# Optimization experiments

Measured on AMD Instinct MI355X. Metric: run time of the kernel, lower is better.

## Reference

```python
import jax, jax.numpy as jnp
import numpy as np

D = 512
H = 8
DK = D // H
EXP = 2
EPS = 1e-5


def _layernorm(x, g, b):
    mu = jnp.mean(x, axis=-1, keepdims=True)
    var = jnp.mean(jnp.square(x - mu), axis=-1, keepdims=True)
    return (x - mu) * jax.lax.rsqrt(var + EPS) * g + b


def setup_inputs() -> dict:
    key = jax.random.key(0)
    ks = jax.random.split(key, 10)
    B, C = 4, 2048
    s = 0.02
    return {
        "h": jax.random.normal(ks[0], (B, C, D), jnp.float32),
        "adj_bias": jax.random.normal(ks[1], (B, C, C), jnp.float32),
        "w_qkv": jax.random.normal(ks[2], (D, 3 * D), jnp.float32) * s,
        "b_qkv": jnp.zeros((3 * D,), jnp.float32),
        "w_out": jax.random.normal(ks[3], (D, D), jnp.float32) * s,
        "b_out": jnp.zeros((D,), jnp.float32),
        "ln1_g": jnp.ones((D,), jnp.float32),
        "ln1_b": jnp.zeros((D,), jnp.float32),
        "ln2_g": jnp.ones((D,), jnp.float32),
        "ln2_b": jnp.zeros((D,), jnp.float32),
        "w1": jax.random.normal(ks[4], (D, D * EXP), jnp.float32) * s,
        "b1": jnp.zeros((D * EXP,), jnp.float32),
        "w2": jax.random.normal(ks[5], (D * EXP, D), jnp.float32) * s,
        "b2": jnp.zeros((D,), jnp.float32),
    }


def reference(h, adj_bias, w_qkv, b_qkv, w_out, b_out, ln1_g, ln1_b, ln2_g, ln2_b, w1, b1, w2, b2):
    B, C, _ = h.shape
    scale = DK ** -0.5
    h_n = _layernorm(h, ln1_g, ln1_b)
    qkv = (h_n @ w_qkv + b_qkv).reshape(B, C, 3, H, DK)
    q, k, v = (qkv[:, :, i].transpose(0, 2, 1, 3) for i in range(3))  # (B,H,C,DK)
    logits = jnp.einsum('bhqd,bhkd->bhqk', q, k) * scale + adj_bias[:, None, :, :]
    attn = jax.nn.softmax(logits, axis=-1)  # (B,H,C,C); dropout off (eval)
    out = jnp.einsum('bhqk,bhkd->bhqd', attn, v).transpose(0, 2, 1, 3).reshape(B, C, D)
    h = h + out @ w_out + b_out
    ff = _layernorm(h, ln2_g, ln2_b)
    ff = jax.nn.gelu(ff @ w1 + b1, approximate=False) @ w2 + b2
    return h + ff
```

## Files before the change

### kernel.cpp

```cpp
#include <hip/hip_runtime.h>
#include <hip/hip_bf16.h>

#define BDIM 4
#define CDIM 2048
#define DDIM 512
#define HH   8
#define DKH  64
#define NROW (BDIM * CDIM)

typedef unsigned short u16;
typedef unsigned int   u32;
typedef u16   u16x4  __attribute__((ext_vector_type(4)));
typedef u16   u16x8  __attribute__((ext_vector_type(8)));
typedef u32   u32x4  __attribute__((ext_vector_type(4)));
typedef __bf16 bf16x8 __attribute__((ext_vector_type(8)));
typedef __bf16 bf16x2 __attribute__((ext_vector_type(2)));
typedef float f32x4  __attribute__((ext_vector_type(4)));
typedef float f32x16 __attribute__((ext_vector_type(16)));

#define LOG2E 1.4426950408889634f

__device__ __forceinline__ u16 f2bf(float f) {
  union { float f; unsigned u; } x; x.f = f;
  unsigned u = x.u;
  u += 0x7fffu + ((u >> 16) & 1u);
  return (u16)(u >> 16);
}
__device__ __forceinline__ float bf2f(u16 u) {
  return __builtin_bit_cast(float, (u32)u << 16);
}
__device__ __forceinline__ u32 pk2(float a, float b) {
  bf16x2 t; t[0] = (__bf16)a; t[1] = (__bf16)b;
  return __builtin_bit_cast(u32, t);
}
__device__ __forceinline__ float fexp2(float x) {
  float r;
  asm("v_exp_f32 %0, %1" : "=v"(r) : "v"(x));
  return r;
}

__device__ __forceinline__ void gload_lds16(const u16* gp, u16* lp) {
  __builtin_amdgcn_global_load_lds((__attribute__((address_space(1))) const void*)gp,
                                   (__attribute__((address_space(3))) void*)lp, 16, 0, 0);
}

__device__ __forceinline__ void ln_body(int bx, int tid,
                                        const float* __restrict__ x,
                                        const float* __restrict__ gamma,
                                        const float* __restrict__ beta,
                                        u16* __restrict__ y) {
  int gw = (bx * 256 + tid) >> 6;
  int l  = tid & 63;
  const float* xr = x + (size_t)gw * DDIM;
  float4 a = *(const float4*)(xr + l * 8);
  float4 b = *(const float4*)(xr + l * 8 + 4);
  float s = a.x + a.y + a.z + a.w + b.x + b.y + b.z + b.w;
  float q = a.x*a.x + a.y*a.y + a.z*a.z + a.w*a.w + b.x*b.x + b.y*b.y + b.z*b.z + b.w*b.w;
#pragma unroll
  for (int m = 1; m < 64; m <<= 1) { s += __shfl_xor(s, m); q += __shfl_xor(q, m); }
  float mu  = s * (1.0f / DDIM);
  float var = q * (1.0f / DDIM) - mu * mu;
  float rs  = rsqrtf(var + 1e-5f);
  float4 g0 = *(const float4*)(gamma + l * 8);
  float4 g1 = *(const float4*)(gamma + l * 8 + 4);
  float4 b0 = *(const float4*)(beta + l * 8);
  float4 b1 = *(const float4*)(beta + l * 8 + 4);
  u16x8 o;
  o[0] = f2bf((a.x - mu) * rs * g0.x + b0.x);
  o[1] = f2bf((a.y - mu) * rs * g0.y + b0.y);
  o[2] = f2bf((a.z - mu) * rs * g0.z + b0.z);
  o[3] = f2bf((a.w - mu) * rs * g0.w + b0.w);
  o[4] = f2bf((b.x - mu) * rs * g1.x + b1.x);
  o[5] = f2bf((b.y - mu) * rs * g1.y + b1.y);
  o[6] = f2bf((b.z - mu) * rs * g1.z + b1.z);
  o[7] = f2bf((b.w - mu) * rs * g1.w + b1.w);
  *(u16x8*)(y + (size_t)gw * DDIM + l * 8) = o;
}

__global__ __launch_bounds__(256) void ln_kernel(const float* __restrict__ x,
                                                 const float* __restrict__ gamma,
                                                 const float* __restrict__ beta,
                                                 u16* __restrict__ y) {
  ln_body(blockIdx.x, threadIdx.x, x, gamma, beta, y);
}

__global__ __launch_bounds__(256) void setup_kernel(const float* __restrict__ h,
                                                    const float* __restrict__ ln1g,
                                                    const float* __restrict__ ln1b,
                                                    u16* __restrict__ hn,
                                                    const float* __restrict__ adj,
                                                    u16* __restrict__ adjC,
                                                    const float* __restrict__ wqkv,
                                                    const float* __restrict__ wout,
                                                    const float* __restrict__ w1,
                                                    const float* __restrict__ w2,
                                                    u16* __restrict__ o_qkv,
                                                    u16* __restrict__ o_out,
                                                    u16* __restrict__ o_w1,
                                                    u16* __restrict__ o_w2) {
  const int bx = blockIdx.x;
  const int t = threadIdx.x;
  if (bx < 2048) {
    ln_body(bx, t, h, ln1g, ln1b, hn);
  } else if (bx < 3072) {
    const int f = bx - 2048;
    const int b = f >> 8, kt = (f >> 3) & 31;
    const int q0 = (f & 7) * 256;
    const int ch = t & 7, c16 = ch & 3, hi2 = ch >> 2, m = c16 >> 1;
    const int K0 = m * 32 + ((c16 * 2) & 3) * 8 + hi2 * 4;
#pragma unroll
    for (int itq = 0; itq < 8; ++itq) {
      int q = q0 + itq * 32 + (t >> 3);
      const float* src = adj + ((size_t)b * CDIM + q) * CDIM + kt * 64;
      f32x4 v0 = *(const f32x4*)(src + K0);
      f32x4 v1 = *(const f32x4*)(src + K0 + 8);
      u16x8 o;
      o[0] = f2bf(v0[0] * LOG2E); o[1] = f2bf(v0[1] * LOG2E);
      o[2] = f2bf(v0[2] * LOG2E); o[3] = f2bf(v0[3] * LOG2E);
      o[4] = f2bf(v1[0] * LOG2E); o[5] = f2bf(v1[1] * LOG2E);
      o[6] = f2bf(v1[2] * LOG2E); o[7] = f2bf(v1[3] * LOG2E);
      *(u16x8*)(adjC + ((size_t)(b * 32 + kt) * 2048 + q) * 64 + ch * 8) = o;
    }
  } else {
    int idx = (bx - 3072) * 256 + t;
    const float* w; u16* wt; int K, N;
    if (idx < 98304)       { w = wqkv; wt = o_qkv; K = 512;  N = 1536; }
    else if (idx < 131072) { idx -= 98304;  w = wout; wt = o_out; K = 512;  N = 512; }
    else if (idx < 196608) { idx -= 131072; w = w1;   wt = o_w1;  K = 512;  N = 1024; }
    else                   { idx -= 196608; w = w2;   wt = o_w2;  K = 1024; N = 512; }
    int kb = K >> 3;
    int n = idx / kb, k0 = (idx - n * kb) * 8;
    u16x8 o;
#pragma unroll
    for (int j = 0; j < 8; ++j) o[j] = f2bf(w[(size_t)(k0 + j) * N + n]);
    *(u16x8*)(wt + (size_t)n * K + k0) = o;
  }
}

template <int EPI>
__device__ __forceinline__ void gemm_epi(int row, int col, float val, int N,
                                         const float* __restrict__ res,
                                         float* __restrict__ outf,
                                         u16* __restrict__ outb,
                                         u16* __restrict__ outq,
                                         u16* __restrict__ outk,
                                         u16* __restrict__ outv) {
  if constexpr (EPI == 0) {
    int t = col >> 9, hh = (col >> 6) & 7, dk = col & 63;
    int bb = row >> 11, cc = row & 2047;
    if (t == 0) {
      val *= 0.125f * LOG2E;
      outq[(((size_t)bb * HH + hh) * CDIM + cc) * DKH + dk] = f2bf(val);
    } else if (t == 1) {
      outk[(((size_t)bb * HH + hh) * CDIM + cc) * DKH + dk] = f2bf(val);
    } else {
      outv[(((size_t)bb * HH + hh) * DKH + dk) * CDIM + cc] = f2bf(val);
    }
  } else if constexpr (EPI == 1) {
    size_t idx = (size_t)row * N + col;
    outf[idx] = val + res[idx];
  } else {
    float g = 0.5f * val * (1.0f + erff(val * 0.70710678118f));
    outb[(size_t)row * N + col] = f2bf(g);
  }
}

template <int EPI>
__global__ __launch_bounds__(256) void gemm128(const u16* __restrict__ A,
                                               const u16* __restrict__ Bt,
                                               const float* __restrict__ bias,
                                               const float* __restrict__ res,
                                               float* __restrict__ outf,
                                               u16* __restrict__ outb,
                                               u16* __restrict__ outq,
                                               u16* __restrict__ outk,
                                               u16* __restrict__ outv,
                                               int M, int N, int K) {
  __shared__ u16 As[2][128 * 64];
  __shared__ u16 Bs[2][128 * 64];
  const int tid = threadIdx.x;
  const int w = tid >> 6, l = tid & 63;
  const int l15 = l & 15, l4 = l >> 4, l7 = l15 & 7;
  const int bm = blockIdx.y, bn = blockIdx.x;
  const int wr = w >> 1, wc = w & 1;

  f32x4 acc[4][4] = {};

  const int sg = (l & 7) ^ (l >> 3);
  const u16* Ag = A  + (size_t)(bm * 128 + w * 32 + (l >> 3)) * K + sg * 8;
  const u16* Bg = Bt + (size_t)(bn * 128 + w * 32 + (l >> 3)) * K + sg * 8;

  auto stage = [&](int buf, int k0) {
#pragma unroll
    for (int i = 0; i < 4; ++i) {
      gload_lds16(Ag + (size_t)(8 * i) * K + k0, &As[buf][(w * 32 + 8 * i) * 64]);
      gload_lds16(Bg + (size_t)(8 * i) * K + k0, &Bs[buf][(w * 32 + 8 * i) * 64]);
    }
  };

  stage(0, 0);
  __syncthreads();
  int cur = 0;
  for (int k0 = 0; k0 < K; k0 += 64) {
    if (k0 + 64 < K) stage(cur ^ 1, k0 + 64);
#pragma unroll
    for (int s = 0; s < 2; ++s) {
      bf16x8 af[4], bf[4];
#pragma unroll
      for (int m = 0; m < 4; ++m)
        af[m] = *(const bf16x8*)(&As[cur][(wr * 64 + m * 16 + l15) * 64 + (((s * 4 + l4) ^ l7) * 8)]);
#pragma unroll
      for (int n = 0; n < 4; ++n)
        bf[n] = *(const bf16x8*)(&Bs[cur][(wc * 64 + n * 16 + l15) * 64 + (((s * 4 + l4) ^ l7) * 8)]);
#pragma unroll
      for (int m = 0; m < 4; ++m)
#pragma unroll
        for (int n = 0; n < 4; ++n)
          acc[m][n] = __builtin_amdgcn_mfma_f32_16x16x32_bf16(af[m], bf[n], acc[m][n], 0, 0, 0);
    }
    __syncthreads();
    cur ^= 1;
  }

#pragma unroll
  for (int m = 0; m < 4; ++m) {
    const int row0 = bm * 128 + wr * 64 + m * 16 + l4 * 4;
#pragma unroll
    for (int n = 0; n < 4; ++n) {
      const int col = bn * 128 + wc * 64 + n * 16 + l15;
      const float bv = bias[col];
#pragma unroll
      for (int r = 0; r < 4; ++r)
        gemm_epi<EPI>(row0 + r, col, acc[m][n][r] + bv, N, res, outf, outb, outq, outk, outv);
    }
  }
}

template <int EPI>
__global__ __launch_bounds__(256) void gemm64(const u16* __restrict__ A,
                                              const u16* __restrict__ Bt,
                                              const float* __restrict__ bias,
                                              const float* __restrict__ res,
                                              float* __restrict__ outf,
                                              u16* __restrict__ outb,
                                              u16* __restrict__ outq,
                                              u16* __restrict__ outk,
                                              u16* __restrict__ outv,
                                              int M, int N, int K) {
  __shared__ u16 As[2][64 * 64];
  __shared__ u16 Bs[2][128 * 64];
  const int tid = threadIdx.x;
  const int w = tid >> 6, l = tid & 63;
  const int l15 = l & 15, l4 = l >> 4, l7 = l15 & 7;
  const int bm = blockIdx.y, bn = blockIdx.x;

  f32x4 acc[4][2] = {};

  const int sg = (l & 7) ^ (l >> 3);
  const u16* Ag = A  + (size_t)(bm * 64  + w * 16 + (l >> 3)) * K + sg * 8;
  const u16* Bg = Bt + (size_t)(bn * 128 + w * 32 + (l >> 3)) * K + sg * 8;

  auto stage = [&](int buf, int k0) {
    gload_lds16(Ag + k0,                  &As[buf][(w * 16 + 0) * 64]);
    gload_lds16(Ag + (size_t)8 * K + k0,  &As[buf][(w * 16 + 8) * 64]);
    gload_lds16(Bg + k0,                  &Bs[buf][(w * 32 + 0) * 64]);
    gload_lds16(Bg + (size_t)8 * K + k0,  &Bs[buf][(w * 32 + 8) * 64]);
    gload_lds16(Bg + (size_t)16 * K + k0, &Bs[buf][(w * 32 + 16) * 64]);
    gload_lds16(Bg + (size_t)24 * K + k0, &Bs[buf][(w * 32 + 24) * 64]);
  };

  stage(0, 0);
  __syncthreads();
  int cur = 0;
  for (int k0 = 0; k0 < K; k0 += 64) {
    if (k0 + 64 < K) stage(cur ^ 1, k0 + 64);
#pragma unroll
    for (int s = 0; s < 2; ++s) {
      bf16x8 af[4], bf[2];
#pragma unroll
      for (int m = 0; m < 4; ++m)
        af[m] = *(const bf16x8*)(&As[cur][(m * 16 + l15) * 64 + (((s * 4 + l4) ^ l7) * 8)]);
#pragma unroll
      for (int n = 0; n < 2; ++n)
        bf[n] = *(const bf16x8*)(&Bs[cur][(w * 32 + n * 16 + l15) * 64 + (((s * 4 + l4) ^ l7) * 8)]);
#pragma unroll
      for (int m = 0; m < 4; ++m)
#pragma unroll
        for (int n = 0; n < 2; ++n)
          acc[m][n] = __builtin_amdgcn_mfma_f32_16x16x32_bf16(af[m], bf[n], acc[m][n], 0, 0, 0);
    }
    __syncthreads();
    cur ^= 1;
  }

#pragma unroll
  for (int m = 0; m < 4; ++m) {
    const int row0 = bm * 64 + m * 16 + l4 * 4;
#pragma unroll
    for (int n = 0; n < 2; ++n) {
      const int col = bn * 128 + w * 32 + n * 16 + l15;
      const float bv = bias[col];
#pragma unroll
      for (int r = 0; r < 4; ++r)
        gemm_epi<EPI>(row0 + r, col, acc[m][n][r] + bv, N, res, outf, outb, outq, outk, outv);
    }
  }
}

__global__ __launch_bounds__(512, 2) void flash_attn(const u16* __restrict__ Q,
                                                     const u16* __restrict__ Kg,
                                                     const u16* __restrict__ Vt,
                                                     const u16* __restrict__ adjC,
                                                     u16* __restrict__ O) {
  __shared__ u16 Ks[2][2][64 * 64];
  __shared__ u16 Vs[2][2][64 * 64];
  __shared__ float lw[4][32];
  __shared__ float lsx[4][32];
  const int flat = blockIdx.x + 16 * blockIdx.y;
  const int virt = (flat & 7) * 64 + (flat >> 3);
  const int qt = virt & 15;
  const int bh = virt >> 4;
  const int b = bh >> 3, hh = bh & 7;
  const int tid = threadIdx.x;
  const int w = tid >> 6, l = tid & 63;
  const int kh = w >> 2, qg = w & 3;
  const int q32 = l & 31, hi = l >> 5;
  const int qglob = qt * 128 + qg * 32 + q32;

  const u16* Qb = Q  + (size_t)bh * CDIM * DKH;
  const u16* Kb = Kg + (size_t)bh * CDIM * DKH;
  const u16* Vb = Vt + (size_t)bh * DKH * CDIM;

  const int srow = qg * 16 + (l >> 3);
  const int sg   = (l & 7) ^ (l >> 3);
  const u16* Kg0 = Kb + (size_t)(srow + 0) * DKH + sg * 8;
  const u16* Kg1 = Kb + (size_t)(srow + 8) * DKH + sg * 8;
  const u16* Vg0 = Vb + (size_t)(srow + 0) * CDIM + sg * 8;
  const u16* Vg1 = Vb + (size_t)(srow + 8) * CDIM + sg * 8;

  bf16x8 qf[4];
#pragma unroll
  for (int s = 0; s < 4; ++s)
    qf[s] = *(const bf16x8*)(Qb + (size_t)qglob * DKH + s * 16 + hi * 8);

  const u16* adjQ = adjC + ((size_t)(b * 32) * 2048 + qglob) * 64 + hi * 32;

  f32x16 oa[2] = {};
  float lsum = 0.f;

  auto stage = [&](int buf, int ktr) {
    int kta = kh * 16 + ktr;
    gload_lds16(Kg0 + (size_t)kta * 4096, &Ks[kh][buf][(qg * 16 + 0) * 64]);
    gload_lds16(Kg1 + (size_t)kta * 4096, &Ks[kh][buf][(qg * 16 + 8) * 64]);
    gload_lds16(Vg0 + kta * 64, &Vs[kh][buf][(qg * 16 + 0) * 64]);
    gload_lds16(Vg1 + kta * 64, &Vs[kh][buf][(qg * 16 + 8) * 64]);
  };
  auto ajload = [&](u16x8* dst, int ktr) {
    const u16* p = adjQ + (size_t)(kh * 16 + ktr) * 131072;
#pragma unroll
    for (int i = 0; i < 4; ++i) dst[i] = *(const u16x8*)(p + i * 8);
  };
  auto computeQK = [&](const u16* KsB, const u16x8* av, f32x16* sa) {
#pragma unroll
    for (int m = 0; m < 2; ++m)
#pragma unroll
      for (int r = 0; r < 16; ++r)
        sa[m][r] = bf2f(av[m * 2 + (r >> 3)][r & 7]);
    __builtin_amdgcn_s_setprio(1);
#pragma unroll
    for (int s = 0; s < 4; ++s)
#pragma unroll
      for (int m = 0; m < 2; ++m) {
        bf16x8 kf = *(const bf16x8*)(&KsB[(m * 32 + q32) * 64 + (((s * 2 + hi) ^ (q32 & 7)) * 8)]);
        sa[m] = __builtin_amdgcn_mfma_f32_32x32x16_bf16(kf, qf[s], sa[m], 0, 0, 0);
      }
    __builtin_amdgcn_s_setprio(0);
  };
  auto computePV = [&](const u16* VsB, f32x16* sa) {
#pragma unroll
    for (int m = 0; m < 2; ++m)
#pragma unroll
      for (int r = 0; r < 16; ++r) {
        float p = fexp2(sa[m][r]);
        sa[m][r] = p;
        lsum += p;
      }
    bf16x8 af[4];
#pragma unroll
    for (int m = 0; m < 2; ++m)
#pragma unroll
      for (int t2 = 0; t2 < 2; ++t2) {
        u32 w0 = pk2(sa[m][t2 * 8 + 0], sa[m][t2 * 8 + 1]);
        u32 w1 = pk2(sa[m][t2 * 8 + 2], sa[m][t2 * 8 + 3]);
        u32 w2 = pk2(sa[m][t2 * 8 + 4], sa[m][t2 * 8 + 5]);
        u32 w3 = pk2(sa[m][t2 * 8 + 6], sa[m][t2 * 8 + 7]);
        auto r02 = __builtin_amdgcn_permlane32_swap(w0, w2, false, false);
        auto r13 = __builtin_amdgcn_permlane32_swap(w1, w3, false, false);
        u32x4 aw;
        aw[0] = r02[0];
        aw[1] = r13[0];
        aw[2] = r02[1];
        aw[3] = r13[1];
        af[m * 2 + t2] = __builtin_bit_cast(bf16x8, aw);
      }
    __builtin_amdgcn_s_setprio(1);
#pragma unroll
    for (int s = 0; s < 4; ++s)
#pragma unroll
      for (int n = 0; n < 2; ++n) {
        bf16x8 vf = *(const bf16x8*)(&VsB[(n * 32 + q32) * 64 + (((s * 2 + hi) ^ (q32 & 7)) * 8)]);
        oa[n] = __builtin_amdgcn_mfma_f32_32x32x16_bf16(af[s], vf, oa[n], 0, 0, 0);
      }
    __builtin_amdgcn_s_setprio(0);
  };

  u16x8 avA[4], avB[4];
  f32x16 sa[2];
  stage(0, 0);
  ajload(avA, 0);
  __syncthreads();
#pragma unroll 1
  for (int it = 0; it < 8; ++it) {
    int ktr = it * 2;
    stage(1, ktr + 1);
    computeQK(&Ks[kh][0][0], avA, sa);
    ajload(avB, ktr + 1);
    computePV(&Vs[kh][0][0], sa);
    __syncthreads();
    if (ktr + 2 < 16) stage(0, ktr + 2);
    computeQK(&Ks[kh][1][0], avB, sa);
    if (ktr + 2 < 16) ajload(avA, ktr + 2);
    computePV(&Vs[kh][1][0], sa);
    __syncthreads();
  }

  lsum += __shfl_xor(lsum, 32);

  float* cb = (float*)&Vs[0][0][0];
  if (kh == 1) {
#pragma unroll
    for (int n = 0; n < 2; ++n)
#pragma unroll
      for (int r = 0; r < 16; ++r)
        cb[((qg * 2 + n) * 16 + r) * 64 + l] = oa[n][r];
    if (hi == 0) lsx[qg][q32] = lsum;
  }
  __syncthreads();
  if (kh == 0) {
    lsum += lsx[qg][q32];
#pragma unroll
    for (int n = 0; n < 2; ++n)
#pragma unroll
      for (int r = 0; r < 16; ++r)
        oa[n][r] += cb[((qg * 2 + n) * 16 + r) * 64 + l];
    lw[qg][q32] = 1.0f / lsum;
#pragma unroll
    for (int n = 0; n < 2; ++n)
#pragma unroll
      for (int r = 0; r < 16; ++r) {
        int qloc = (r & 3) + 8 * (r >> 2) + 4 * hi;
        int row = qt * 128 + qg * 32 + qloc;
        float val = oa[n][r] * lw[qg][qloc];
        O[((size_t)b * CDIM + row) * DDIM + hh * 64 + n * 32 + q32] = f2bf(val);
      }
  }
}

extern "C" void kernel_launch(void* const* d_in, const int* in_sizes, int n_in,
                              void* d_out, int out_size, void* d_ws, size_t ws_size,
                              hipStream_t stream) {
  const float* h      = (const float*)d_in[0];
  const float* adj    = (const float*)d_in[1];
  const float* w_qkv  = (const float*)d_in[2];
  const float* b_qkv  = (const float*)d_in[3];
  const float* w_out  = (const float*)d_in[4];
  const float* b_out  = (const float*)d_in[5];
  const float* ln1g   = (const float*)d_in[6];
  const float* ln1b   = (const float*)d_in[7];
  const float* ln2g   = (const float*)d_in[8];
  const float* ln2b   = (const float*)d_in[9];
  const float* w1     = (const float*)d_in[10];
  const float* b1     = (const float*)d_in[11];
  const float* w2     = (const float*)d_in[12];
  const float* b2     = (const float*)d_in[13];
  float* out = (float*)d_out;

  char* ws = (char*)d_ws;
  u16* adjC  = (u16*)(ws);
  u16* hn    = (u16*)(ws + 33554432);
  u16* qb    = (u16*)(ws + 41943040);
  u16* kb    = (u16*)(ws + 50331648);
  u16* vt    = (u16*)(ws + 58720256);
  u16* attn  = (u16*)(ws + 67108864);
  u16* wqkvt = (u16*)(ws + 75497472);
  u16* woutt = (u16*)(ws + 77070336);
  u16* w1t   = (u16*)(ws + 77594624);
  u16* w2t   = (u16*)(ws + 78643200);
  u16* ffin  = hn;
  u16* ffmid = qb;

  setup_kernel<<<4096, 256, 0, stream>>>(h, ln1g, ln1b, hn, adj, adjC,
                                         w_qkv, w_out, w1, w2,
                                         wqkvt, woutt, w1t, w2t);

  gemm128<0><<<dim3(12, 64), 256, 0, stream>>>(hn, wqkvt, b_qkv, nullptr,
                                               nullptr, nullptr, qb, kb, vt,
                                               NROW, 3 * DDIM, DDIM);

  flash_attn<<<dim3(16, 32), 512, 0, stream>>>(qb, kb, vt, adjC, attn);

  gemm64<1><<<dim3(4, 128), 256, 0, stream>>>(attn, woutt, b_out, h,
                                              out, nullptr, nullptr, nullptr, nullptr,
                                              NROW, DDIM, DDIM);

  ln_kernel<<<2048, 256, 0, stream>>>(out, ln2g, ln2b, ffin);

  gemm128<2><<<dim3(8, 64), 256, 0, stream>>>(ffin, w1t, b1, nullptr,
                                              nullptr, ffmid, nullptr, nullptr, nullptr,
                                              NROW, 2 * DDIM, DDIM);

  gemm64<1><<<dim3(4, 128), 256, 0, stream>>>(ffmid, w2t, b2, out,
                                              out, nullptr, nullptr, nullptr, nullptr,
                                              NROW, DDIM, 2 * DDIM);
}
```

Before: 192.4 us.

## Drop split-K in flash attention and add XCD-aware block remap to GEMMs

The attention kernel no longer splits the key range across two wave groups. Each 256-thread block now walks all 32 key tiles itself, which removes the cross-half LDS reduction and the extra barrier, halves shared memory, and raises the occupancy target. The normalisation factor is broadcast with a shuffle instead of going through LDS. Separately, the GEMM kernels remap block indices so that neighbouring tiles land on the same XCD for better L2 reuse. The trade-off is half as many waves per block and a longer serial loop per block.

```diff
diff --git a/kernel.cpp b/kernel.cpp
--- a/kernel.cpp
+++ b/kernel.cpp
@@ -165,6 +165,15 @@
   }
 }
 
+__device__ __forceinline__ void xcd_remap(int& bn, int& bm) {
+  int nbn = gridDim.x;
+  int nwg = nbn * gridDim.y;
+  int flat = blockIdx.x + nbn * blockIdx.y;
+  int virt = (flat & 7) * (nwg >> 3) + (flat >> 3);
+  bn = virt % nbn;
+  bm = virt / nbn;
+}
+
 template <int EPI>
 __global__ __launch_bounds__(256) void gemm128(const u16* __restrict__ A,
                                                const u16* __restrict__ Bt,
@@ -181,7 +190,8 @@
   const int tid = threadIdx.x;
   const int w = tid >> 6, l = tid & 63;
   const int l15 = l & 15, l4 = l >> 4, l7 = l15 & 7;
-  const int bm = blockIdx.y, bn = blockIdx.x;
+  int bn, bm;
+  xcd_remap(bn, bm);
   const int wr = w >> 1, wc = w & 1;
 
   f32x4 acc[4][4] = {};
@@ -252,7 +262,8 @@
   const int tid = threadIdx.x;
   const int w = tid >> 6, l = tid & 63;
   const int l15 = l & 15, l4 = l >> 4, l7 = l15 & 7;
-  const int bm = blockIdx.y, bn = blockIdx.x;
+  int bn, bm;
+  xcd_remap(bn, bm);
 
   f32x4 acc[4][2] = {};
 
@@ -307,15 +318,13 @@
   }
 }
 
-__global__ __launch_bounds__(512, 2) void flash_attn(const u16* __restrict__ Q,
+__global__ __launch_bounds__(256, 5) void flash_attn(const u16* __restrict__ Q,
                                                      const u16* __restrict__ Kg,
                                                      const u16* __restrict__ Vt,
                                                      const u16* __restrict__ adjC,
                                                      u16* __restrict__ O) {
-  __shared__ u16 Ks[2][2][64 * 64];
-  __shared__ u16 Vs[2][2][64 * 64];
-  __shared__ float lw[4][32];
-  __shared__ float lsx[4][32];
+  __shared__ u16 Ks[2][64 * 64];
+  __shared__ u16 Vs[2][64 * 64];
   const int flat = blockIdx.x + 16 * blockIdx.y;
   const int virt = (flat & 7) * 64 + (flat >> 3);
   const int qt = virt & 15;
@@ -323,7 +332,7 @@
   const int b = bh >> 3, hh = bh & 7;
   const int tid = threadIdx.x;
   const int w = tid >> 6, l = tid & 63;
-  const int kh = w >> 2, qg = w & 3;
+  const int qg = w;
   const int q32 = l & 31, hi = l >> 5;
   const int qglob = qt * 128 + qg * 32 + q32;
 
@@ -348,15 +357,14 @@
   f32x16 oa[2] = {};
   float lsum = 0.f;
 
-  auto stage = [&](int buf, int ktr) {
-    int kta = kh * 16 + ktr;
-    gload_lds16(Kg0 + (size_t)kta * 4096, &Ks[kh][buf][(qg * 16 + 0) * 64]);
-    gload_lds16(Kg1 + (size_t)kta * 4096, &Ks[kh][buf][(qg * 16 + 8) * 64]);
-    gload_lds16(Vg0 + kta * 64, &Vs[kh][buf][(qg * 16 + 0) * 64]);
-    gload_lds16(Vg1 + kta * 64, &Vs[kh][buf][(qg * 16 + 8) * 64]);
+  auto stage = [&](int buf, int kt) {
+    gload_lds16(Kg0 + (size_t)kt * 4096, &Ks[buf][(qg * 16 + 0) * 64]);
+    gload_lds16(Kg1 + (size_t)kt * 4096, &Ks[buf][(qg * 16 + 8) * 64]);
+    gload_lds16(Vg0 + kt * 64, &Vs[buf][(qg * 16 + 0) * 64]);
+    gload_lds16(Vg1 + kt * 64, &Vs[buf][(qg * 16 + 8) * 64]);
   };
-  auto ajload = [&](u16x8* dst, int ktr) {
-    const u16* p = adjQ + (size_t)(kh * 16 + ktr) * 131072;
+  auto ajload = [&](u16x8* dst, int kt) {
+    const u16* p = adjQ + (size_t)kt * 131072;
 #pragma unroll
     for (int i = 0; i < 4; ++i) dst[i] = *(const u16x8*)(p + i * 8);
   };
@@ -420,50 +428,32 @@
   ajload(avA, 0);
   __syncthreads();
 #pragma unroll 1
-  for (int it = 0; it < 8; ++it) {
-    int ktr = it * 2;
-    stage(1, ktr + 1);
-    computeQK(&Ks[kh][0][0], avA, sa);
-    ajload(avB, ktr + 1);
-    computePV(&Vs[kh][0][0], sa);
+  for (int it = 0; it < 16; ++it) {
+    int kt = it * 2;
+    stage(1, kt + 1);
+    computeQK(&Ks[0][0], avA, sa);
+    ajload(avB, kt + 1);
+    computePV(&Vs[0][0], sa);
     __syncthreads();
-    if (ktr + 2 < 16) stage(0, ktr + 2);
-    computeQK(&Ks[kh][1][0], avB, sa);
-    if (ktr + 2 < 16) ajload(avA, ktr + 2);
-    computePV(&Vs[kh][1][0], sa);
+    if (kt + 2 < 32) stage(0, kt + 2);
+    computeQK(&Ks[1][0], avB, sa);
+    if (kt + 2 < 32) ajload(avA, kt + 2);
+    computePV(&Vs[1][0], sa);
     __syncthreads();
   }
 
   lsum += __shfl_xor(lsum, 32);
-
-  float* cb = (float*)&Vs[0][0][0];
-  if (kh == 1) {
-#pragma unroll
-    for (int n = 0; n < 2; ++n)
-#pragma unroll
-      for (int r = 0; r < 16; ++r)
-        cb[((qg * 2 + n) * 16 + r) * 64 + l] = oa[n][r];
-    if (hi == 0) lsx[qg][q32] = lsum;
-  }
-  __syncthreads();
-  if (kh == 0) {
-    lsum += lsx[qg][q32];
-#pragma unroll
-    for (int n = 0; n < 2; ++n)
-#pragma unroll
-      for (int r = 0; r < 16; ++r)
-        oa[n][r] += cb[((qg * 2 + n) * 16 + r) * 64 + l];
-    lw[qg][q32] = 1.0f / lsum;
-#pragma unroll
-    for (int n = 0; n < 2; ++n)
-#pragma unroll
-      for (int r = 0; r < 16; ++r) {
-        int qloc = (r & 3) + 8 * (r >> 2) + 4 * hi;
-        int row = qt * 128 + qg * 32 + qloc;
-        float val = oa[n][r] * lw[qg][qloc];
-        O[((size_t)b * CDIM + row) * DDIM + hh * 64 + n * 32 + q32] = f2bf(val);
-      }
-  }
+  float inv = 1.0f / lsum;
+
+#pragma unroll
+  for (int n = 0; n < 2; ++n)
+#pragma unroll
+    for (int r = 0; r < 16; ++r) {
+      int qloc = (r & 3) + 8 * (r >> 2) + 4 * hi;
+      float invr = __shfl(inv, (l & 32) | qloc);
+      int row = qt * 128 + qg * 32 + qloc;
+      O[((size_t)b * CDIM + row) * DDIM + hh * 64 + n * 32 + q32] = f2bf(oa[n][r] * invr);
+    }
 }
 
 extern "C" void kernel_launch(void* const* d_in, const int* in_sizes, int n_in,
@@ -507,7 +497,7 @@
                                                nullptr, nullptr, qb, kb, vt,
                                                NROW, 3 * DDIM, DDIM);
 
-  flash_attn<<<dim3(16, 32), 512, 0, stream>>>(qb, kb, vt, adjC, attn);
+  flash_attn<<<dim3(16, 32), 256, 0, stream>>>(qb, kb, vt, adjC, attn);
 
   gemm64<1><<<dim3(4, 128), 256, 0, stream>>>(attn, woutt, b_out, h,
                                               out, nullptr, nullptr, nullptr, nullptr,
```

Measured after the change: 405.7 us. 111% more time.

## Move adjacency conversion into QKV GEMM launch and remap workgroups for XCD locality

Applied to the files above, without the earlier changes.

The adjacency-bias bf16 conversion moves out of the setup kernel and into a combined kernel that runs the QKV GEMM tiles and the adj conversion blocks in one launch. The memory-bound conversion can then overlap with the compute-bound GEMM. All GEMM kernels also remap the flat block index so consecutive tiles land on the same XCD (stride-8 interleave), which should improve L2 reuse of A/B tiles. Risks: LDS usage in the fused kernel limits occupancy for the adj blocks, and the remap assumes the workgroup count is divisible by 8.

```diff
diff --git a/kernel.cpp b/kernel.cpp
--- a/kernel.cpp
+++ b/kernel.cpp
@@ -84,12 +84,32 @@
   ln_body(blockIdx.x, threadIdx.x, x, gamma, beta, y);
 }
 
+__device__ __forceinline__ void adj_body(int f, int t,
+                                         const float* __restrict__ adj,
+                                         u16* __restrict__ adjC) {
+  const int b = f >> 8, kt = (f >> 3) & 31;
+  const int q0 = (f & 7) * 256;
+  const int ch = t & 7, c16 = ch & 3, hi2 = ch >> 2, m = c16 >> 1;
+  const int K0 = m * 32 + ((c16 * 2) & 3) * 8 + hi2 * 4;
+#pragma unroll
+  for (int itq = 0; itq < 8; ++itq) {
+    int q = q0 + itq * 32 + (t >> 3);
+    const float* src = adj + ((size_t)b * CDIM + q) * CDIM + kt * 64;
+    f32x4 v0 = *(const f32x4*)(src + K0);
+    f32x4 v1 = *(const f32x4*)(src + K0 + 8);
+    u16x8 o;
+    o[0] = f2bf(v0[0] * LOG2E); o[1] = f2bf(v0[1] * LOG2E);
+    o[2] = f2bf(v0[2] * LOG2E); o[3] = f2bf(v0[3] * LOG2E);
+    o[4] = f2bf(v1[0] * LOG2E); o[5] = f2bf(v1[1] * LOG2E);
+    o[6] = f2bf(v1[2] * LOG2E); o[7] = f2bf(v1[3] * LOG2E);
+    *(u16x8*)(adjC + ((size_t)(b * 32 + kt) * 2048 + q) * 64 + ch * 8) = o;
+  }
+}
+
 __global__ __launch_bounds__(256) void setup_kernel(const float* __restrict__ h,
                                                     const float* __restrict__ ln1g,
                                                     const float* __restrict__ ln1b,
                                                     u16* __restrict__ hn,
-                                                    const float* __restrict__ adj,
-                                                    u16* __restrict__ adjC,
                                                     const float* __restrict__ wqkv,
                                                     const float* __restrict__ wout,
                                                     const float* __restrict__ w1,
@@ -102,27 +122,8 @@
   const int t = threadIdx.x;
   if (bx < 2048) {
     ln_body(bx, t, h, ln1g, ln1b, hn);
-  } else if (bx < 3072) {
-    const int f = bx - 2048;
-    const int b = f >> 8, kt = (f >> 3) & 31;
-    const int q0 = (f & 7) * 256;
-    const int ch = t & 7, c16 = ch & 3, hi2 = ch >> 2, m = c16 >> 1;
-    const int K0 = m * 32 + ((c16 * 2) & 3) * 8 + hi2 * 4;
-#pragma unroll
-    for (int itq = 0; itq < 8; ++itq) {
-      int q = q0 + itq * 32 + (t >> 3);
-      const float* src = adj + ((size_t)b * CDIM + q) * CDIM + kt * 64;
-      f32x4 v0 = *(const f32x4*)(src + K0);
-      f32x4 v1 = *(const f32x4*)(src + K0 + 8);
-      u16x8 o;
-      o[0] = f2bf(v0[0] * LOG2E); o[1] = f2bf(v0[1] * LOG2E);
-      o[2] = f2bf(v0[2] * LOG2E); o[3] = f2bf(v0[3] * LOG2E);
-      o[4] = f2bf(v1[0] * LOG2E); o[5] = f2bf(v1[1] * LOG2E);
-      o[6] = f2bf(v1[2] * LOG2E); o[7] = f2bf(v1[3] * LOG2E);
-      *(u16x8*)(adjC + ((size_t)(b * 32 + kt) * 2048 + q) * 64 + ch * 8) = o;
-    }
   } else {
-    int idx = (bx - 3072) * 256 + t;
+    int idx = (bx - 2048) * 256 + t;
     const float* w; u16* wt; int K, N;
     if (idx < 98304)       { w = wqkv; wt = o_qkv; K = 512;  N = 1536; }
     else if (idx < 131072) { idx -= 98304;  w = wout; wt = o_out; K = 512;  N = 512; }
@@ -166,22 +167,24 @@
 }
 
 template <int EPI>
-__global__ __launch_bounds__(256) void gemm128(const u16* __restrict__ A,
-                                               const u16* __restrict__ Bt,
-                                               const float* __restrict__ bias,
-                                               const float* __restrict__ res,
-                                               float* __restrict__ outf,
-                                               u16* __restrict__ outb,
-                                               u16* __restrict__ outq,
-                                               u16* __restrict__ outk,
-                                               u16* __restrict__ outv,
-                                               int M, int N, int K) {
+__device__ __forceinline__ void gemm128_body(int flat, int nbn, int nwg,
+                                             const u16* __restrict__ A,
+                                             const u16* __restrict__ Bt,
+                                             const float* __restrict__ bias,
+                                             const float* __restrict__ res,
+                                             float* __restrict__ outf,
+                                             u16* __restrict__ outb,
+                                             u16* __restrict__ outq,
+                                             u16* __restrict__ outk,
+                                             u16* __restrict__ outv,
+                                             int N, int K) {
   __shared__ u16 As[2][128 * 64];
   __shared__ u16 Bs[2][128 * 64];
   const int tid = threadIdx.x;
   const int w = tid >> 6, l = tid & 63;
   const int l15 = l & 15, l4 = l >> 4, l7 = l15 & 7;
-  const int bm = blockIdx.y, bn = blockIdx.x;
+  const int virt = (flat & 7) * (nwg >> 3) + (flat >> 3);
+  const int bn = virt % nbn, bm = virt / nbn;
   const int wr = w >> 1, wc = w & 1;
 
   f32x4 acc[4][4] = {};
@@ -234,6 +237,35 @@
         gemm_epi<EPI>(row0 + r, col, acc[m][n][r] + bv, N, res, outf, outb, outq, outk, outv);
     }
   }
+}
+
+__global__ __launch_bounds__(256) void qkv_adj_kernel(const u16* __restrict__ A,
+                                                      const u16* __restrict__ Bt,
+                                                      const float* __restrict__ bias,
+                                                      u16* __restrict__ outq,
+                                                      u16* __restrict__ outk,
+                                                      u16* __restrict__ outv,
+                                                      const float* __restrict__ adj,
+                                                      u16* __restrict__ adjC) {
+  if (blockIdx.x < 768) {
+    gemm128_body<0>(blockIdx.x, 12, 768, A, Bt, bias, nullptr,
+                    nullptr, nullptr, outq, outk, outv, 3 * DDIM, DDIM);
+  } else {
+    adj_body(blockIdx.x - 768, threadIdx.x, adj, adjC);
+  }
+}
+
+template <int EPI>
+__global__ __launch_bounds__(256) void gemm128k(const u16* __restrict__ A,
+                                                const u16* __restrict__ Bt,
+                                                const float* __restrict__ bias,
+                                                const float* __restrict__ res,
+                                                float* __restrict__ outf,
+                                                u16* __restrict__ outb,
+                                                int M, int N, int K) {
+  gemm128_body<EPI>(blockIdx.x + gridDim.x * blockIdx.y, gridDim.x,
+                    gridDim.x * gridDim.y, A, Bt, bias, res,
+                    outf, outb, nullptr, nullptr, nullptr, N, K);
 }
 
 template <int EPI>
@@ -243,16 +275,16 @@
                                               const float* __restrict__ res,
                                               float* __restrict__ outf,
                                               u16* __restrict__ outb,
-                                              u16* __restrict__ outq,
-                                              u16* __restrict__ outk,
-                                              u16* __restrict__ outv,
                                               int M, int N, int K) {
   __shared__ u16 As[2][64 * 64];
   __shared__ u16 Bs[2][128 * 64];
   const int tid = threadIdx.x;
   const int w = tid >> 6, l = tid & 63;
   const int l15 = l & 15, l4 = l >> 4, l7 = l15 & 7;
-  const int bm = blockIdx.y, bn = blockIdx.x;
+  const int nbn = gridDim.x, nwg = gridDim.x * gridDim.y;
+  const int flat = blockIdx.x + nbn * blockIdx.y;
+  const int virt = (flat & 7) * (nwg >> 3) + (flat >> 3);
+  const int bn = virt % nbn, bm = virt / nbn;
 
   f32x4 acc[4][2] = {};
 
@@ -302,7 +334,8 @@
       const float bv = bias[col];
 #pragma unroll
       for (int r = 0; r < 4; ++r)
-        gemm_epi<EPI>(row0 + r, col, acc[m][n][r] + bv, N, res, outf, outb, outq, outk, outv);
+        gemm_epi<EPI>(row0 + r, col, acc[m][n][r] + bv, N, res, outf, outb,
+                      nullptr, nullptr, nullptr);
     }
   }
 }
@@ -499,27 +532,23 @@
   u16* ffin  = hn;
   u16* ffmid = qb;
 
-  setup_kernel<<<4096, 256, 0, stream>>>(h, ln1g, ln1b, hn, adj, adjC,
+  setup_kernel<<<3072, 256, 0, stream>>>(h, ln1g, ln1b, hn,
                                          w_qkv, w_out, w1, w2,
                                          wqkvt, woutt, w1t, w2t);
 
-  gemm128<0><<<dim3(12, 64), 256, 0, stream>>>(hn, wqkvt, b_qkv, nullptr,
-                                               nullptr, nullptr, qb, kb, vt,
-                                               NROW, 3 * DDIM, DDIM);
+  qkv_adj_kernel<<<1792, 256, 0, stream>>>(hn, wqkvt, b_qkv, qb, kb, vt,
+                                           adj, adjC);
 
   flash_attn<<<dim3(16, 32), 512, 0, stream>>>(qb, kb, vt, adjC, attn);
 
   gemm64<1><<<dim3(4, 128), 256, 0, stream>>>(attn, woutt, b_out, h,
-                                              out, nullptr, nullptr, nullptr, nullptr,
-                                              NROW, DDIM, DDIM);
+                                              out, nullptr, NROW, DDIM, DDIM);
 
   ln_kernel<<<2048, 256, 0, stream>>>(out, ln2g, ln2b, ffin);
 
-  gemm128<2><<<dim3(8, 64), 256, 0, stream>>>(ffin, w1t, b1, nullptr,
-                                              nullptr, ffmid, nullptr, nullptr, nullptr,
-                                              NROW, 2 * DDIM, DDIM);
+  gemm128k<2><<<dim3(8, 64), 256, 0, stream>>>(ffin, w1t, b1, nullptr,
+                                               nullptr, ffmid, NROW, 2 * DDIM, DDIM);
 
   gemm64<1><<<dim3(4, 128), 256, 0, stream>>>(ffmid, w2t, b2, out,
-                                              out, nullptr, nullptr, nullptr, nullptr,
-                                              NROW, DDIM, 2 * DDIM);
-}
+                                              out, nullptr, NROW, DDIM, 2 * DDIM);
+}
```

Result: faster. 181.8 us (-5.5%).
